# Performance work log

Measured on AMD Instinct MI355X. Metric: run time of the kernel, lower is better.

Reference implementation:

```python
import jax, jax.numpy as jnp
import numpy as np

SEQ_LEN = 4096
EMB = 2048
INP = 457  # totalSyscalls + 1


def setup_inputs() -> dict:
    key = jax.random.key(0)
    ks = jax.random.split(key, 11)
    s_e = 1.0 / np.sqrt(EMB)  # torch LSTM init scale: 1/sqrt(hidden_size)
    s_d = 1.0 / np.sqrt(INP)
    u = lambda k, shape, s: jax.random.uniform(k, shape, jnp.float32, -s, s)
    return {
        "x": jax.random.normal(ks[0], (1, SEQ_LEN, INP), jnp.float32),
        # Encoder LSTM: input_size=INP, hidden_size=EMB
        "enc_Wih": u(ks[1], (4 * EMB, INP), s_e),
        "enc_Whh": u(ks[2], (4 * EMB, EMB), s_e),
        "enc_bih": u(ks[3], (4 * EMB,), s_e),
        "enc_bhh": u(ks[4], (4 * EMB,), s_e),
        # Decoder LSTM: input_size=EMB, hidden_size=INP, proj_size=EMB
        "dec_Wih": u(ks[5], (4 * INP, EMB), s_d),
        "dec_Whh": u(ks[6], (4 * INP, EMB), s_d),
        "dec_bih": u(ks[7], (4 * INP,), s_d),
        "dec_bhh": u(ks[8], (4 * INP,), s_d),
        "dec_Whr": u(ks[9], (EMB, INP), s_d),
    }


def reference(x, enc_Wih, enc_Whh, enc_bih, enc_bhh,
              dec_Wih, dec_Whh, dec_bih, dec_bhh, dec_Whr):
    xs = x.reshape(SEQ_LEN, INP)  # batch dim is structurally 1

    # ---- Encoder: standard LSTM scanned over timesteps (torch gate order i,f,g,o)
    def enc_step(carry, xt):
        h, c = carry
        g = xt @ enc_Wih.T + enc_bih + h @ enc_Whh.T + enc_bhh  # (4*EMB,)
        i, f, gg, o = jnp.split(g, 4)
        c = jax.nn.sigmoid(f) * c + jax.nn.sigmoid(i) * jnp.tanh(gg)
        h = jax.nn.sigmoid(o) * jnp.tanh(c)
        return (h, c), None

    z = jnp.zeros(EMB, x.dtype)
    (h_enc, _), _ = jax.lax.scan(enc_step, (z, z), xs)

    # ---- Decoder: LSTM with projection (hidden_size=INP, proj_size=EMB),
    # feeds its own projected output back in; collects CELL states each step,
    # prepended (torch.cat([cells, out], 0)) => reversed chronological order.
    def dec_step(carry, _):
        xd, h, c = carry
        g = xd @ dec_Wih.T + dec_bih + h @ dec_Whh.T + dec_bhh  # (4*INP,)
        i, f, gg, o = jnp.split(g, 4)
        c = jax.nn.sigmoid(f) * c + jax.nn.sigmoid(i) * jnp.tanh(gg)
        h_raw = jax.nn.sigmoid(o) * jnp.tanh(c)  # (INP,)
        h = h_raw @ dec_Whr.T                     # projected hidden (EMB,)
        return (h, h, c), c

    init = (h_enc, jnp.zeros(EMB, x.dtype), jnp.zeros(INP, x.dtype))
    _, cells = jax.lax.scan(dec_step, init, None, length=SEQ_LEN)  # (SEQ_LEN, INP)
    out = cells[::-1]
    return jax.nn.softmax(out, axis=1)
```

## Files before the change

### kernel.cpp

```cpp
#include <hip/hip_runtime.h>
#include <cmath>

#define SEQ 4096
#define INP 457
#define EMB 2048
#define NWG_E 256
#define NWG_D 16

typedef unsigned long long u64t;
typedef float f32x4 __attribute__((ext_vector_type(4)));
typedef float f32x2 __attribute__((ext_vector_type(2)));

__device__ __forceinline__ float sigf(float v) { return 1.0f / (1.0f + expf(-v)); }

#define PIN(v) asm volatile("" : "+v"(v))

#define QNAN __builtin_bit_cast(float, 0x7fc00000u)

__device__ __forceinline__ f32x4 poll16(const f32x4* p) {
  f32x4 v;
  asm volatile("global_load_dwordx4 %0, %1, off sc0 sc1\n\ts_waitcnt vmcnt(0)"
               : "=v"(v) : "v"(p) : "memory");
  return v;
}
__device__ __forceinline__ f32x2 poll8(const f32x2* p) {
  f32x2 v;
  asm volatile("global_load_dwordx2 %0, %1, off sc0 sc1\n\ts_waitcnt vmcnt(0)"
               : "=v"(v) : "v"(p) : "memory");
  return v;
}

__global__ void bias_kernel(const float* __restrict__ ebih, const float* __restrict__ ebhh,
                            const float* __restrict__ dbih, const float* __restrict__ dbhh,
                            float* __restrict__ bsum, float* __restrict__ btot) {
  int i = blockIdx.x * 256 + threadIdx.x;
  if (i < 4 * EMB) bsum[i] = ebih[i] + ebhh[i];
  if (i < 4 * INP) btot[i] = dbih[i] + dbhh[i];
}

__global__ __launch_bounds__(256) void fold_gemm(const float* __restrict__ dWih,
                                                 const float* __restrict__ dWhh,
                                                 const float* __restrict__ dWhr,
                                                 float* __restrict__ C) {
  const int bx = blockIdx.x, by = blockIdx.y;
  const int tid = threadIdx.x;
  const int tx = tid & 15, ty = tid >> 4;
  __shared__ float As[16][65];
  __shared__ float Bs[16][65];
  float acc[4][4] = {};
  for (int k0 = 0; k0 < EMB; k0 += 16) {
#pragma unroll
    for (int e = 0; e < 4; ++e) {
      int eid = tid * 4 + e;
      int m = eid >> 4, k = eid & 15;
      int row = by * 64 + m;
      float v = 0.0f;
      if (row < 4 * INP) {
        size_t a = (size_t)row * EMB + k0 + k;
        v = dWih[a] + dWhh[a];
      }
      As[k][m] = v;
    }
#pragma unroll
    for (int e = 0; e < 4; ++e) {
      int eid = tid * 4 + e;
      int k = eid >> 6, c = eid & 63;
      int col = bx * 64 + c;
      Bs[k][c] = (col < INP) ? dWhr[(size_t)(k0 + k) * INP + col] : 0.0f;
    }
    __syncthreads();
#pragma unroll
    for (int k = 0; k < 16; ++k) {
      float a0 = As[k][ty * 4 + 0], a1 = As[k][ty * 4 + 1], a2 = As[k][ty * 4 + 2], a3 = As[k][ty * 4 + 3];
      float b0 = Bs[k][tx * 4 + 0], b1 = Bs[k][tx * 4 + 1], b2 = Bs[k][tx * 4 + 2], b3 = Bs[k][tx * 4 + 3];
      acc[0][0] += a0 * b0; acc[0][1] += a0 * b1; acc[0][2] += a0 * b2; acc[0][3] += a0 * b3;
      acc[1][0] += a1 * b0; acc[1][1] += a1 * b1; acc[1][2] += a1 * b2; acc[1][3] += a1 * b3;
      acc[2][0] += a2 * b0; acc[2][1] += a2 * b1; acc[2][2] += a2 * b2; acc[2][3] += a2 * b3;
      acc[3][0] += a3 * b0; acc[3][1] += a3 * b1; acc[3][2] += a3 * b2; acc[3][3] += a3 * b3;
    }
    __syncthreads();
  }
#pragma unroll
  for (int i = 0; i < 4; ++i) {
    int row = by * 64 + ty * 4 + i;
    if (row >= 4 * INP) continue;
#pragma unroll
    for (int j = 0; j < 4; ++j) {
      int col = bx * 64 + tx * 4 + j;
      if (col < 480) C[(size_t)row * 480 + col] = acc[i][j];
    }
  }
}

__global__ __launch_bounds__(512) __attribute__((amdgpu_waves_per_eu(2, 2))) void enc_kernel(
    const float* __restrict__ x, const float* __restrict__ Wih,
    const float* __restrict__ Whh, const float* __restrict__ bsum,
    float* __restrict__ hbuf) {
  const int tid = threadIdx.x;
  const int wg  = blockIdx.x;
  const int j   = tid & 7;
  const int kc  = tid >> 3;
  const int jbase = wg * 8;

  float wh[4][32];
  float wi[4][8];
#pragma unroll
  for (int g = 0; g < 4; ++g) {
    const size_t row = (size_t)(g * EMB + jbase + j);
    const float* wp = Whh + row * EMB + kc * 32;
#pragma unroll
    for (int q = 0; q < 8; ++q) {
      const float4 v = *(const float4*)(wp + 4 * q);
      wh[g][q * 4 + 0] = v.x; wh[g][q * 4 + 1] = v.y;
      wh[g][q * 4 + 2] = v.z; wh[g][q * 4 + 3] = v.w;
    }
    const float* ip = Wih + row * INP;
#pragma unroll
    for (int i = 0; i < 8; ++i) {
      const int c = kc * 8 + i;
      wi[g][i] = (c < INP) ? ip[c] : 0.0f;
    }
  }
#pragma unroll
  for (int g = 0; g < 4; ++g) {
#pragma unroll
    for (int q = 0; q < 32; ++q) PIN(wh[g][q]);
#pragma unroll
    for (int q = 0; q < 8; ++q) PIN(wi[g][q]);
  }

  __shared__ float4 hl4[512];
  __shared__ float4 xl4[128];
  __shared__ float  partbuf[256];
  __shared__ float  b_s[32];
  __shared__ float  c_s[8];
  if (tid < 32) b_s[tid] = bsum[(tid >> 3) * EMB + jbase + (tid & 7)];
  if (tid < 8)  c_s[tid] = 0.0f;
  const int sw = kc & 7;
  const int hphys = tid ^ ((tid >> 3) & 7);
  const int xi = (tid < INP) ? tid : 0;

  for (int t = 0; t < SEQ; ++t) {
    const float xraw = x[(size_t)t * INP + xi];

    const f32x4* gp = (const f32x4*)(hbuf + (size_t)(t & 3) * EMB) + tid;
    f32x4 g4;
    for (;;) {
      g4 = poll16(gp);
      if ((g4.x == g4.x) & (g4.y == g4.y) & (g4.z == g4.z) & (g4.w == g4.w)) break;
    }
    hl4[hphys] = make_float4(g4.x, g4.y, g4.z, g4.w);
    ((float*)xl4)[tid] = (tid < INP) ? xraw : 0.0f;

    float4 a0 = make_float4(0, 0, 0, 0), a1 = a0, a2 = a0, a3 = a0;
#pragma unroll
    for (int q = 0; q < 2; ++q) {
      const float4 xq = xl4[kc * 2 + q];
      a0.x += wi[0][q * 4 + 0] * xq.x; a0.y += wi[0][q * 4 + 1] * xq.y; a0.z += wi[0][q * 4 + 2] * xq.z; a0.w += wi[0][q * 4 + 3] * xq.w;
      a1.x += wi[1][q * 4 + 0] * xq.x; a1.y += wi[1][q * 4 + 1] * xq.y; a1.z += wi[1][q * 4 + 2] * xq.z; a1.w += wi[1][q * 4 + 3] * xq.w;
      a2.x += wi[2][q * 4 + 0] * xq.x; a2.y += wi[2][q * 4 + 1] * xq.y; a2.z += wi[2][q * 4 + 2] * xq.z; a2.w += wi[2][q * 4 + 3] * xq.w;
      a3.x += wi[3][q * 4 + 0] * xq.x; a3.y += wi[3][q * 4 + 1] * xq.y; a3.z += wi[3][q * 4 + 2] * xq.z; a3.w += wi[3][q * 4 + 3] * xq.w;
    }
#pragma unroll
    for (int q = 0; q < 8; ++q) {
      const float4 hv = hl4[kc * 8 + (q ^ sw)];
      const int b = q * 4;
      a0.x += wh[0][b + 0] * hv.x; a0.y += wh[0][b + 1] * hv.y; a0.z += wh[0][b + 2] * hv.z; a0.w += wh[0][b + 3] * hv.w;
      a1.x += wh[1][b + 0] * hv.x; a1.y += wh[1][b + 1] * hv.y; a1.z += wh[1][b + 2] * hv.z; a1.w += wh[1][b + 3] * hv.w;
      a2.x += wh[2][b + 0] * hv.x; a2.y += wh[2][b + 1] * hv.y; a2.z += wh[2][b + 2] * hv.z; a2.w += wh[2][b + 3] * hv.w;
      a3.x += wh[3][b + 0] * hv.x; a3.y += wh[3][b + 1] * hv.y; a3.z += wh[3][b + 2] * hv.z; a3.w += wh[3][b + 3] * hv.w;
    }

    float r0 = (a0.x + a0.y) + (a0.z + a0.w);
    float r1 = (a1.x + a1.y) + (a1.z + a1.w);
    float r2 = (a2.x + a2.y) + (a2.z + a2.w);
    float r3 = (a3.x + a3.y) + (a3.z + a3.w);
#pragma unroll
    for (int m = 8; m < 64; m <<= 1) {
      r0 += __shfl_xor(r0, m); r1 += __shfl_xor(r1, m);
      r2 += __shfl_xor(r2, m); r3 += __shfl_xor(r3, m);
    }
    if ((tid & 63) < 8)
      *(float4*)(partbuf + (tid >> 6) * 32 + j * 4) = make_float4(r0, r1, r2, r3);
    __syncthreads();

    if (tid < 8) {
      __hip_atomic_store(hbuf + (size_t)((t + 3) & 3) * EMB + jbase + tid, QNAN,
                         __ATOMIC_RELAXED, __HIP_MEMORY_SCOPE_AGENT);
      float s0 = 0.f, s1 = 0.f, s2 = 0.f, s3 = 0.f;
#pragma unroll
      for (int w = 0; w < 8; ++w) {
        const float4 pv = *(const float4*)(partbuf + w * 32 + tid * 4);
        s0 += pv.x; s1 += pv.y; s2 += pv.z; s3 += pv.w;
      }
      const float gi = s0 + b_s[tid], gf = s1 + b_s[8 + tid];
      const float gg = s2 + b_s[16 + tid], go = s3 + b_s[24 + tid];
      const float cN = sigf(gf) * c_s[tid] + sigf(gi) * tanhf(gg);
      c_s[tid] = cN;
      const float hN = sigf(go) * tanhf(cN);
      asm volatile("s_waitcnt vmcnt(0)" ::: "memory");
      __hip_atomic_store(hbuf + (size_t)((t + 1) & 3) * EMB + jbase + tid, hN,
                         __ATOMIC_RELAXED, __HIP_MEMORY_SCOPE_AGENT);
    }
  }
}

__global__ __launch_bounds__(512) __attribute__((amdgpu_waves_per_eu(2, 2))) void dec_kernel(
    const float* __restrict__ dWih, const float* __restrict__ Wfold,
    const float* __restrict__ btot, const float* __restrict__ henc,
    float* __restrict__ hraw, float* __restrict__ out) {
  const int tid = threadIdx.x;
  const int wg  = blockIdx.x;
  const int j   = tid & 31;
  const int kc  = tid >> 5;
  const int idx = wg * 32 + j;
  const bool valid = (idx < INP);
  const int id0 = valid ? idx : 0;
  const int l   = tid & 63;
  const int wv  = tid >> 6;
  int gl = l;
  if (gl >= 30) gl -= 30;
  if (gl >= 30) gl -= 30;
  const int gidx = 30 * wv + gl;

  float wd[4][30];
#pragma unroll
  for (int g = 0; g < 4; ++g) {
    const float* wp = Wfold + (size_t)(g * INP + id0) * 480 + kc * 30;
#pragma unroll
    for (int q = 0; q < 15; ++q) {
      const float2 v = valid ? *(const float2*)(wp + 2 * q) : make_float2(0.0f, 0.0f);
      wd[g][q * 2 + 0] = v.x; wd[g][q * 2 + 1] = v.y;
    }
  }
#pragma unroll
  for (int g = 0; g < 4; ++g)
#pragma unroll
    for (int q = 0; q < 30; ++q) PIN(wd[g][q]);

  __shared__ float2 dl2[240];
  __shared__ float  partbuf[1024];
  __shared__ float  b_s[128];
  __shared__ float  c_s[32];
  if (tid < 128) {
    const int ix = wg * 32 + (tid & 31);
    b_s[tid] = (ix < INP) ? btot[(tid >> 5) * INP + ix] : 0.0f;
  }
  if (tid < 32) c_s[tid] = 0.0f;

  for (int t = 0; t < SEQ; ++t) {
    if (t > 0) {
      const f32x2* gp = (const f32x2*)(hraw + (size_t)(t & 3) * 512) + gidx;
      f32x2 g2;
      for (;;) {
        g2 = poll8(gp);
        if ((g2.x == g2.x) & (g2.y == g2.y)) break;
      }
      if (l < 30) dl2[gidx] = make_float2(g2.x, g2.y);
    }

    float2 acc0 = make_float2(0, 0), acc1 = acc0, acc2 = acc0, acc3 = acc0;
    if (t == 0) {
      if (valid) {
#pragma unroll 4
        for (int q = 0; q < 32; ++q) {
          const float4 hv = *(const float4*)(henc + kc * 128 + 4 * q);
          const float4 w0 = *(const float4*)(dWih + (size_t)(0 * INP + idx) * EMB + kc * 128 + 4 * q);
          const float4 w1 = *(const float4*)(dWih + (size_t)(1 * INP + idx) * EMB + kc * 128 + 4 * q);
          const float4 w2 = *(const float4*)(dWih + (size_t)(2 * INP + idx) * EMB + kc * 128 + 4 * q);
          const float4 w3 = *(const float4*)(dWih + (size_t)(3 * INP + idx) * EMB + kc * 128 + 4 * q);
          acc0.x += w0.x * hv.x + w0.z * hv.z; acc0.y += w0.y * hv.y + w0.w * hv.w;
          acc1.x += w1.x * hv.x + w1.z * hv.z; acc1.y += w1.y * hv.y + w1.w * hv.w;
          acc2.x += w2.x * hv.x + w2.z * hv.z; acc2.y += w2.y * hv.y + w2.w * hv.w;
          acc3.x += w3.x * hv.x + w3.z * hv.z; acc3.y += w3.y * hv.y + w3.w * hv.w;
        }
      }
    } else {
#pragma unroll
      for (int q = 0; q < 15; ++q) {
        const float2 hv = dl2[kc * 15 + q];
        acc0.x += wd[0][q * 2] * hv.x; acc0.y += wd[0][q * 2 + 1] * hv.y;
        acc1.x += wd[1][q * 2] * hv.x; acc1.y += wd[1][q * 2 + 1] * hv.y;
        acc2.x += wd[2][q * 2] * hv.x; acc2.y += wd[2][q * 2 + 1] * hv.y;
        acc3.x += wd[3][q * 2] * hv.x; acc3.y += wd[3][q * 2 + 1] * hv.y;
      }
    }
    float r0 = acc0.x + acc0.y, r1 = acc1.x + acc1.y, r2 = acc2.x + acc2.y, r3 = acc3.x + acc3.y;
    r0 += __shfl_xor(r0, 32); r1 += __shfl_xor(r1, 32);
    r2 += __shfl_xor(r2, 32); r3 += __shfl_xor(r3, 32);
    if ((tid & 63) < 32)
      *(float4*)(partbuf + (tid >> 6) * 128 + (tid & 31) * 4) = make_float4(r0, r1, r2, r3);
    __syncthreads();

    if (tid < 32) {
      const int ix = wg * 32 + tid;
      if (ix < 480)
        __hip_atomic_store(hraw + (size_t)((t + 3) & 3) * 512 + ix, QNAN,
                           __ATOMIC_RELAXED, __HIP_MEMORY_SCOPE_AGENT);
      float s0 = 0.f, s1 = 0.f, s2 = 0.f, s3 = 0.f;
#pragma unroll
      for (int w = 0; w < 8; ++w) {
        const float4 pv = *(const float4*)(partbuf + w * 128 + tid * 4);
        s0 += pv.x; s1 += pv.y; s2 += pv.z; s3 += pv.w;
      }
      const float gi = s0 + b_s[tid], gf = s1 + b_s[32 + tid];
      const float gg = s2 + b_s[64 + tid], go = s3 + b_s[96 + tid];
      const float cN = sigf(gf) * c_s[tid] + sigf(gi) * tanhf(gg);
      c_s[tid] = cN;
      const float hrN = sigf(go) * tanhf(cN);
      asm volatile("s_waitcnt vmcnt(0)" ::: "memory");
      if (ix < 480)
        __hip_atomic_store(hraw + (size_t)((t + 1) & 3) * 512 + ix, (ix < INP) ? hrN : 0.0f,
                           __ATOMIC_RELAXED, __HIP_MEMORY_SCOPE_AGENT);
      if (ix < INP) out[(size_t)(SEQ - 1 - t) * INP + ix] = cN;
    }
  }
}

__global__ __launch_bounds__(512) void softmax_kernel(float* __restrict__ out) {
  const int row = blockIdx.x;
  const int tid = threadIdx.x;
  __shared__ float red[512];
  float* rp = out + (size_t)row * INP;
  float v = (tid < INP) ? rp[tid] : -INFINITY;
  red[tid] = v;
  __syncthreads();
#pragma unroll
  for (int off = 256; off > 0; off >>= 1) {
    if (tid < off) red[tid] = fmaxf(red[tid], red[tid + off]);
    __syncthreads();
  }
  const float m = red[0];
  __syncthreads();
  const float e = (tid < INP) ? expf(v - m) : 0.0f;
  red[tid] = e;
  __syncthreads();
#pragma unroll
  for (int off = 256; off > 0; off >>= 1) {
    if (tid < off) red[tid] = red[tid] + red[tid + off];
    __syncthreads();
  }
  const float s = red[0];
  if (tid < INP) rp[tid] = e / s;
}

extern "C" void kernel_launch(void* const* d_in, const int* in_sizes, int n_in,
                              void* d_out, int out_size, void* d_ws, size_t ws_size,
                              hipStream_t stream) {
  const float* x    = (const float*)d_in[0];
  const float* eWih = (const float*)d_in[1];
  const float* eWhh = (const float*)d_in[2];
  const float* ebih = (const float*)d_in[3];
  const float* ebhh = (const float*)d_in[4];
  const float* dWih = (const float*)d_in[5];
  const float* dWhh = (const float*)d_in[6];
  const float* dbih = (const float*)d_in[7];
  const float* dbhh = (const float*)d_in[8];
  const float* dWhr = (const float*)d_in[9];
  float* out = (float*)d_out;
  char* ws = (char*)d_ws;

  float* hbuf  = (float*)(ws + 0);
  float* hraw  = (float*)(ws + 32768);
  float* bsum  = (float*)(ws + 40960);
  float* btot  = (float*)(ws + 73728);
  float* Wfold = (float*)(ws + 81920);

  hipMemsetAsync(ws, 0xFF, 40960, stream);
  hipMemsetAsync(ws, 0x00, 8192, stream);
  bias_kernel<<<40, 256, 0, stream>>>(ebih, ebhh, dbih, dbhh, bsum, btot);
  fold_gemm<<<dim3(8, 29), 256, 0, stream>>>(dWih, dWhh, dWhr, Wfold);
  enc_kernel<<<NWG_E, 512, 0, stream>>>(x, eWih, eWhh, bsum, hbuf);
  dec_kernel<<<NWG_D, 512, 0, stream>>>(dWih, Wfold, btot, hbuf, hraw, out);
  softmax_kernel<<<SEQ, 512, 0, stream>>>(out);
}
```

Before: 19.01 ms.

## Replace NaN-sentinel polling in encoder with atomic step counters

```diff
diff --git a/kernel.cpp b/kernel.cpp
--- a/kernel.cpp
+++ b/kernel.cpp
@@ -10,6 +10,7 @@
 typedef unsigned long long u64t;
 typedef float f32x4 __attribute__((ext_vector_type(4)));
 typedef float f32x2 __attribute__((ext_vector_type(2)));
+typedef unsigned u32x4 __attribute__((ext_vector_type(4)));
 
 __device__ __forceinline__ float sigf(float v) { return 1.0f / (1.0f + expf(-v)); }
 
@@ -17,13 +18,19 @@
 
 #define QNAN __builtin_bit_cast(float, 0x7fc00000u)
 
-__device__ __forceinline__ f32x4 poll16(const f32x4* p) {
+__device__ __forceinline__ f32x4 mall16(const f32x4* p) {
   f32x4 v;
   asm volatile("global_load_dwordx4 %0, %1, off sc0 sc1\n\ts_waitcnt vmcnt(0)"
                : "=v"(v) : "v"(p) : "memory");
   return v;
 }
-__device__ __forceinline__ f32x2 poll8(const f32x2* p) {
+__device__ __forceinline__ u32x4 mall16u(const u32x4* p) {
+  u32x4 v;
+  asm volatile("global_load_dwordx4 %0, %1, off sc0 sc1\n\ts_waitcnt vmcnt(0)"
+               : "=v"(v) : "v"(p) : "memory");
+  return v;
+}
+__device__ __forceinline__ f32x2 mall8(const f32x2* p) {
   f32x2 v;
   asm volatile("global_load_dwordx2 %0, %1, off sc0 sc1\n\ts_waitcnt vmcnt(0)"
                : "=v"(v) : "v"(p) : "memory");
@@ -95,7 +102,7 @@
 __global__ __launch_bounds__(512) __attribute__((amdgpu_waves_per_eu(2, 2))) void enc_kernel(
     const float* __restrict__ x, const float* __restrict__ Wih,
     const float* __restrict__ Whh, const float* __restrict__ bsum,
-    float* __restrict__ hbuf) {
+    float* __restrict__ hbuf, unsigned* __restrict__ cnt) {
   const int tid = threadIdx.x;
   const int wg  = blockIdx.x;
   const int j   = tid & 7;
@@ -143,12 +150,14 @@
   for (int t = 0; t < SEQ; ++t) {
     const float xraw = x[(size_t)t * INP + xi];
 
-    const f32x4* gp = (const f32x4*)(hbuf + (size_t)(t & 3) * EMB) + tid;
-    f32x4 g4;
-    for (;;) {
-      g4 = poll16(gp);
-      if ((g4.x == g4.x) & (g4.y == g4.y) & (g4.z == g4.z) & (g4.w == g4.w)) break;
-    }
+    if (t > 0 && (tid & 63) == 0) {
+      const unsigned tgt = (unsigned)t * 64u;
+      for (;;) {
+        const u32x4 c = mall16u((const u32x4*)cnt);
+        if (c.x >= tgt && c.y >= tgt && c.z >= tgt && c.w >= tgt) break;
+      }
+    }
+    const f32x4 g4 = mall16((const f32x4*)(hbuf + (size_t)(t & 1) * EMB) + tid);
     hl4[hphys] = make_float4(g4.x, g4.y, g4.z, g4.w);
     ((float*)xl4)[tid] = (tid < INP) ? xraw : 0.0f;
 
@@ -185,8 +194,6 @@
     __syncthreads();
 
     if (tid < 8) {
-      __hip_atomic_store(hbuf + (size_t)((t + 3) & 3) * EMB + jbase + tid, QNAN,
-                         __ATOMIC_RELAXED, __HIP_MEMORY_SCOPE_AGENT);
       float s0 = 0.f, s1 = 0.f, s2 = 0.f, s3 = 0.f;
 #pragma unroll
       for (int w = 0; w < 8; ++w) {
@@ -198,9 +205,11 @@
       const float cN = sigf(gf) * c_s[tid] + sigf(gi) * tanhf(gg);
       c_s[tid] = cN;
       const float hN = sigf(go) * tanhf(cN);
+      __hip_atomic_store(hbuf + (size_t)((t + 1) & 1) * EMB + jbase + tid, hN,
+                         __ATOMIC_RELAXED, __HIP_MEMORY_SCOPE_AGENT);
       asm volatile("s_waitcnt vmcnt(0)" ::: "memory");
-      __hip_atomic_store(hbuf + (size_t)((t + 1) & 3) * EMB + jbase + tid, hN,
-                         __ATOMIC_RELAXED, __HIP_MEMORY_SCOPE_AGENT);
+      if (tid == 0)
+        __hip_atomic_fetch_add(cnt + (wg & 3), 1u, __ATOMIC_RELAXED, __HIP_MEMORY_SCOPE_AGENT);
     }
   }
 }
@@ -253,7 +262,7 @@
       const f32x2* gp = (const f32x2*)(hraw + (size_t)(t & 3) * 512) + gidx;
       f32x2 g2;
       for (;;) {
-        g2 = poll8(gp);
+        g2 = mall8(gp);
         if ((g2.x == g2.x) & (g2.y == g2.y)) break;
       }
       if (l < 30) dl2[gidx] = make_float2(g2.x, g2.y);
@@ -362,15 +371,17 @@
 
   float* hbuf  = (float*)(ws + 0);
   float* hraw  = (float*)(ws + 32768);
-  float* bsum  = (float*)(ws + 40960);
-  float* btot  = (float*)(ws + 73728);
-  float* Wfold = (float*)(ws + 81920);
+  unsigned* cnt = (unsigned*)(ws + 40960);
+  float* bsum  = (float*)(ws + 41984);
+  float* btot  = (float*)(ws + 74752);
+  float* Wfold = (float*)(ws + 82944);
 
   hipMemsetAsync(ws, 0xFF, 40960, stream);
   hipMemsetAsync(ws, 0x00, 8192, stream);
+  hipMemsetAsync(ws + 40960, 0x00, 1024, stream);
   bias_kernel<<<40, 256, 0, stream>>>(ebih, ebhh, dbih, dbhh, bsum, btot);
   fold_gemm<<<dim3(8, 29), 256, 0, stream>>>(dWih, dWhh, dWhr, Wfold);
-  enc_kernel<<<NWG_E, 512, 0, stream>>>(x, eWih, eWhh, bsum, hbuf);
+  enc_kernel<<<NWG_E, 512, 0, stream>>>(x, eWih, eWhh, bsum, hbuf, cnt);
   dec_kernel<<<NWG_D, 512, 0, stream>>>(dWih, Wfold, btot, hbuf, hraw, out);
   softmax_kernel<<<SEQ, 512, 0, stream>>>(out);
 }
```

Result: slower. 52.81 ms (+177.9%).
